# Kernel tuning notes

Hardware: AMD Instinct MI355X
Metric: run time of the kernel (lower is better)

Reference implementation:

```python
import jax, jax.numpy as jnp
import numpy as np
import math

RATIO = 16
B, C, H, W = 8, 684, 16, 64
HID, INP, AD, V, T = 256, 256, 512, 111, 36

def conv2d(x, w, b=None, padding=0):
    out = jax.lax.conv_general_dilated(x, w, (1, 1), [(padding, padding)] * 2,
                                       dimension_numbers=('NCHW', 'OIHW', 'NCHW'))
    if b is not None:
        out = out + b[None, :, None, None]
    return out

def pos_embedding_sine(mask, num_pos_feats=256, temperature=10000.0):
    # mask: [B,H,W] float. Normalized sine position embedding -> [B, 2*num_pos_feats, H, W]
    scale = 2.0 * math.pi
    eps = 1e-6
    y = jnp.cumsum(mask, axis=1)
    x = jnp.cumsum(mask, axis=2)
    y = y / (y[:, -1:, :] + eps) * scale
    x = x / (x[:, :, -1:] + eps) * scale
    i = jnp.arange(num_pos_feats, dtype=jnp.float32)
    dim_t = temperature ** (2.0 * jnp.floor(i / 2.0) / num_pos_feats)
    px = x[..., None] / dim_t  # [B,H,W,F]
    py = y[..., None] / dim_t
    def interleave(p):
        return jnp.stack((jnp.sin(p[..., 0::2]), jnp.cos(p[..., 1::2])), axis=4).reshape(p.shape[:3] + (num_pos_feats,))
    pos = jnp.concatenate((interleave(py), interleave(px)), axis=3)
    return jnp.transpose(pos, (0, 3, 1, 2))

def gru_cell(x, h, w_ih, w_hh, b_ih, b_hh):
    gi = x @ w_ih.T + b_ih
    gh = h @ w_hh.T + b_hh
    ir, iz, inn = jnp.split(gi, 3, axis=-1)
    hr, hz, hn = jnp.split(gh, 3, axis=-1)
    r = jax.nn.sigmoid(ir + hr)
    z = jax.nn.sigmoid(iz + hz)
    n = jnp.tanh(inn + r * hn)
    return (1.0 - z) * n + z * h

def setup_inputs() -> dict:
    key = jax.random.key(0)
    ks = jax.random.split(key, 32)
    s = 0.05
    d = {}
    d['cnn_features'] = jax.random.normal(ks[0], (B, C, H, W), jnp.float32)
    d['counting_preds'] = jax.random.uniform(ks[1], (B, V), jnp.float32)
    d['images_mask'] = jnp.ones((B, 1, H * RATIO, W * RATIO), jnp.float32)
    d['init_W'] = jax.random.normal(ks[2], (HID, C), jnp.float32) * s
    d['init_b'] = jax.random.normal(ks[3], (HID,), jnp.float32) * s
    d['emb'] = jax.random.normal(ks[4], (V, INP), jnp.float32) * s
    d['gru_w_ih'] = jax.random.normal(ks[5], (3 * HID, INP), jnp.float32) * s
    d['gru_w_hh'] = jax.random.normal(ks[6], (3 * HID, HID), jnp.float32) * s
    d['gru_b_ih'] = jax.random.normal(ks[7], (3 * HID,), jnp.float32) * s
    d['gru_b_hh'] = jax.random.normal(ks[8], (3 * HID,), jnp.float32) * s
    d['att_hidden_W'] = jax.random.normal(ks[9], (AD, HID), jnp.float32) * s
    d['att_hidden_b'] = jax.random.normal(ks[10], (AD,), jnp.float32) * s
    d['att_conv_w'] = jax.random.normal(ks[11], (512, 1, 11, 11), jnp.float32) * s
    d['att_weight_W'] = jax.random.normal(ks[12], (AD, 512), jnp.float32) * s
    d['alpha_convert_W'] = jax.random.normal(ks[13], (1, AD), jnp.float32) * s
    d['alpha_convert_b'] = jax.random.normal(ks[14], (1,), jnp.float32) * s
    d['enc_conv_w'] = jax.random.normal(ks[15], (AD, C, 1, 1), jnp.float32) * s
    d['enc_conv_b'] = jax.random.normal(ks[16], (AD,), jnp.float32) * s
    d['state_W'] = jax.random.normal(ks[17], (HID, HID), jnp.float32) * s
    d['state_b'] = jax.random.normal(ks[18], (HID,), jnp.float32) * s
    d['embw_W'] = jax.random.normal(ks[19], (HID, INP), jnp.float32) * s
    d['embw_b'] = jax.random.normal(ks[20], (HID,), jnp.float32) * s
    d['ctx_W'] = jax.random.normal(ks[21], (HID, C), jnp.float32) * s
    d['ctx_b'] = jax.random.normal(ks[22], (HID,), jnp.float32) * s
    d['count_W'] = jax.random.normal(ks[23], (HID, V), jnp.float32) * s
    d['count_b'] = jax.random.normal(ks[24], (HID,), jnp.float32) * s
    d['out_W'] = jax.random.normal(ks[25], (V, HID), jnp.float32) * s
    d['out_b'] = jax.random.normal(ks[26], (V,), jnp.float32) * s
    d['labels'] = jax.random.randint(ks[27], (B, T), 1, V)
    return d

def reference(cnn_features, counting_preds, images_mask, init_W, init_b, emb,
              gru_w_ih, gru_w_hh, gru_b_ih, gru_b_hh,
              att_hidden_W, att_hidden_b, att_conv_w, att_weight_W,
              alpha_convert_W, alpha_convert_b, enc_conv_w, enc_conv_b,
              state_W, state_b, embw_W, embw_b, ctx_W, ctx_b,
              count_W, count_b, out_W, out_b, labels):
    b, c, h, w = cnn_features.shape
    dmask = images_mask[:, :, ::RATIO, ::RATIO]  # [B,1,H,W]
    mask_hw = dmask[:, 0]                        # [B,H,W]
    # init hidden
    avg = jnp.sum(cnn_features * dmask, axis=(2, 3)) / jnp.sum(dmask, axis=(2, 3))
    hidden0 = jnp.tanh(avg @ init_W.T + init_b)
    counting_ctx = counting_preds @ count_W.T + count_b  # [B,HID]
    trans = conv2d(cnn_features, enc_conv_w, enc_conv_b)  # [B,AD,H,W], k=1
    trans = trans + pos_embedding_sine(mask_hw)
    trans_hw = jnp.transpose(trans, (0, 2, 3, 1))  # [B,H,W,AD]
    word0 = jnp.ones((b,), dtype=labels.dtype)
    words_in = jnp.concatenate([word0[:, None], labels[:, :-1]], axis=1)  # teacher forcing
    alpha_sum0 = jnp.zeros((b, 1, h, w), cnn_features.dtype)

    def step(carry, word):
        hidden, alpha_sum = carry
        we = emb[word]
        hidden = gru_cell(we, hidden, gru_w_ih, gru_w_hh, gru_b_ih, gru_b_hh)
        query = hidden @ att_hidden_W.T + att_hidden_b          # [B,AD]
        ast = conv2d(alpha_sum, att_conv_w, padding=5)          # [B,512,H,W]
        coverage = jnp.einsum('bchw,dc->bhwd', ast, att_weight_W)
        score = jnp.tanh(query[:, None, None, :] + coverage + trans_hw)
        energy = jnp.einsum('bhwd,d->bhw', score, alpha_convert_W[0]) + alpha_convert_b[0]
        energy = energy - energy.max()
        e = jnp.exp(energy) * mask_hw
        alpha = e / (jnp.sum(e, axis=(1, 2))[:, None, None] + 1e-10)
        alpha_sum = alpha[:, None] + alpha_sum
        ctx = jnp.einsum('bhw,bchw->bc', alpha, cnn_features)
        out_state = (hidden @ state_W.T + state_b
                     + we @ embw_W.T + embw_b
                     + ctx @ ctx_W.T + ctx_b
                     + counting_ctx)
        prob = out_state @ out_W.T + out_b
        return (hidden, alpha_sum), prob

    _, probs = jax.lax.scan(step, (hidden0, alpha_sum0), words_in.T)
    return jnp.transpose(probs, (1, 0, 2))  # [B,T,V]
```

## Files before the change

### kernel.cpp

```cpp
#include <hip/hip_runtime.h>
#include <hip/hip_bf16.h>
#include <math.h>

#define NB 8
#define NC 684
#define NH 16
#define NW 64
#define NHW 1024
#define NHID 256
#define NAD 512
#define NV 111
#define NT 36
#define KPAD 704

typedef __attribute__((ext_vector_type(8))) short bf16x8;
typedef __attribute__((ext_vector_type(4))) float f32x4;

__device__ __forceinline__ float wred_sum(float v){
  #pragma unroll
  for (int o = 32; o > 0; o >>= 1) v += __shfl_xor(v, o, 64);
  return v;
}
__device__ __forceinline__ float wred_max(float v){
  #pragma unroll
  for (int o = 32; o > 0; o >>= 1) v = fmaxf(v, __shfl_xor(v, o, 64));
  return v;
}
__device__ __forceinline__ float fsig(float x){ return 1.f/(1.f + __expf(-x)); }
__device__ __forceinline__ float ftanh(float x){ float e = __expf(2.f*x); return 1.f - 2.f/(e + 1.f); }
__device__ __forceinline__ unsigned short f2bf(float f){
  __hip_bfloat16 h = __float2bfloat16(f);
  return *(unsigned short*)&h;
}
__device__ __forceinline__ float bf2f(unsigned short u){
  return __uint_as_float(((unsigned)u) << 16);
}

__global__ void k_p0(const float* __restrict__ im, float* __restrict__ dmask,
                     float* __restrict__ msum, float* __restrict__ ys, float* __restrict__ xs,
                     float* __restrict__ idt, float* __restrict__ abuf)
{
  const int tid = threadIdx.x;
  for (int i = tid; i < NB*NHW; i += 256){
    int b = i >> 10, hw = i & 1023; int h = hw >> 6, w = hw & 63;
    dmask[i] = im[b*(256*1024) + (h*16)*1024 + (w*16)];
    abuf[i] = 0.f;
  }
  if (tid < 128) idt[tid] = expf(-(float)tid * (9.210340371976184f/128.f));
  __syncthreads();
  if (tid < 8){
    float s = 0.f;
    for (int i = 0; i < NHW; i++) s += dmask[tid*NHW + i];
    msum[tid] = s;
  }
  for (int p = tid; p < NB*NW; p += 256){
    int b = p >> 6, w = p & 63;
    float tot = 0.f;
    for (int h = 0; h < NH; h++) tot += dmask[b*NHW + h*64 + w];
    float inv = 6.283185307179586f/(tot + 1e-6f);
    float run = 0.f;
    for (int h = 0; h < NH; h++){ run += dmask[b*NHW + h*64 + w]; ys[b*NHW + h*64 + w] = run*inv; }
  }
  for (int p = tid; p < NB*NH; p += 256){
    int b = p >> 4, h = p & 15;
    float tot = 0.f;
    for (int w = 0; w < NW; w++) tot += dmask[b*NHW + h*64 + w];
    float inv = 6.283185307179586f/(tot + 1e-6f);
    float run = 0.f;
    for (int w = 0; w < NW; w++){ run += dmask[b*NHW + h*64 + w]; xs[b*NHW + h*64 + w] = run*inv; }
  }
}

__global__ void k_avg(const float* __restrict__ cnn, const float* __restrict__ dmask,
                      const float* __restrict__ msum, float* __restrict__ avg)
{
  int gid = blockIdx.x*blockDim.x + threadIdx.x;
  int gw = gid >> 6, lane = gid & 63;
  int nw = (gridDim.x*blockDim.x) >> 6;
  for (int ow = gw; ow < NB*NC; ow += nw){
    int b = ow / NC;
    const float* base = cnn + (size_t)ow * NHW;
    const float* dm = dmask + b*NHW;
    float s = 0.f;
    for (int i = lane; i < NHW; i += 64) s += base[i]*dm[i];
    s = wred_sum(s);
    if (lane == 0) avg[ow] = s / msum[b];
  }
}

__global__ void k_init(const float* __restrict__ avg, const float* __restrict__ iW, const float* __restrict__ ib,
                       const float* __restrict__ cp, const float* __restrict__ cW, const float* __restrict__ cb,
                       float* __restrict__ hm1, float* __restrict__ cctx)
{
  int gid = blockIdx.x*blockDim.x + threadIdx.x;
  int gw = gid >> 6, lane = gid & 63;
  int nw = (gridDim.x*blockDim.x) >> 6;
  for (int ow = gw; ow < 2*NB*NHID; ow += nw){
    if (ow < NB*NHID){
      int b = ow >> 8, j = ow & 255;
      float s = 0.f;
      for (int k = lane; k < NC; k += 64) s += avg[b*NC + k]*iW[j*NC + k];
      s = wred_sum(s);
      if (lane == 0) hm1[ow] = tanhf(s + ib[j]);
    } else {
      int o = ow - NB*NHID; int b = o >> 8, j = o & 255;
      float s = 0.f;
      for (int k = lane; k < NV; k += 64) s += cp[b*NV + k]*cW[j*NV + k];
      s = wred_sum(s);
      if (lane == 0) cctx[o] = s + cb[j];
    }
  }
}

__global__ __launch_bounds__(256) void k_cvt(const float* __restrict__ cnn, unsigned short* __restrict__ cnnT)
{
  const int hw0 = blockIdx.x << 6, c0 = blockIdx.y << 6, b = blockIdx.z;
  __shared__ float T[64][65];
  const int tid = threadIdx.x;
  #pragma unroll
  for (int u = 0; u < 16; u++){
    int idx = tid + (u<<8);
    int cc = idx >> 6, mm = idx & 63;
    int c = c0 + cc;
    T[cc][mm] = (c < NC) ? cnn[((size_t)b*NC + c)*NHW + hw0 + mm] : 0.f;
  }
  __syncthreads();
  #pragma unroll
  for (int r0 = 0; r0 < 64; r0 += 8){
    int hwl = r0 + (tid >> 5);
    int cp = (tid & 31) << 1;
    unsigned u0 = f2bf(T[cp][hwl]);
    unsigned u1 = f2bf(T[cp+1][hwl]);
    *(unsigned*)&cnnT[((size_t)((b<<10) + hw0 + hwl))*KPAD + c0 + cp] = (u1 << 16) | u0;
  }
}

__global__ void k_cvtw(const float* __restrict__ ew, unsigned short* __restrict__ ewb)
{
  int x = blockIdx.x*256 + threadIdx.x;
  if (x >= NAD*KPAD) return;
  int d = x / KPAD, c = x - d*KPAD;
  float v = (c < NC) ? ew[(size_t)d*NC + c] : 0.f;
  ewb[x] = f2bf(v);
}

__global__ __launch_bounds__(256) void k_mma_trans(const unsigned short* __restrict__ cnnT,
    const unsigned short* __restrict__ ewb, const float* __restrict__ eb,
    const float* __restrict__ ys, const float* __restrict__ xs,
    const float* __restrict__ idt, unsigned short* __restrict__ transb)
{
  const int m0 = blockIdx.x << 7;
  const int n0 = blockIdx.y << 6;
  const int b = m0 >> 10, hw0 = m0 & 1023;
  const int tid = threadIdx.x, lane = tid & 63, wv = tid >> 6;
  const int kgrp = (lane >> 4) << 3;
  const unsigned short* arow0 = cnnT + ((size_t)((b<<10) + hw0 + (wv<<5) + (lane & 15)))*KPAD + kgrp;
  const unsigned short* arow1 = arow0 + (size_t)16*KPAD;
  f32x4 acc[2][4];
  #pragma unroll
  for (int mt=0; mt<2; mt++)
    #pragma unroll
    for (int s = 0; s < 4; s++){ acc[mt][s][0]=0.f; acc[mt][s][1]=0.f; acc[mt][s][2]=0.f; acc[mt][s][3]=0.f; }
  #pragma unroll 2
  for (int k0 = 0; k0 < KPAD; k0 += 32){
    bf16x8 a0 = *(const bf16x8*)(arow0 + k0);
    bf16x8 a1 = *(const bf16x8*)(arow1 + k0);
    #pragma unroll
    for (int s = 0; s < 4; s++){
      const unsigned short* brow = ewb + (size_t)(n0 + (s<<4) + (lane & 15))*KPAD + kgrp + k0;
      bf16x8 bf = *(const bf16x8*)brow;
      acc[0][s] = __builtin_amdgcn_mfma_f32_16x16x32_bf16(a0, bf, acc[0][s], 0, 0, 0);
      acc[1][s] = __builtin_amdgcn_mfma_f32_16x16x32_bf16(a1, bf, acc[1][s], 0, 0, 0);
    }
  }
  #pragma unroll
  for (int mt = 0; mt < 2; mt++){
    #pragma unroll
    for (int r = 0; r < 4; r++){
      int hw = hw0 + (wv<<5) + (mt<<4) + ((lane>>4)<<2) + r;
      float ysv = ys[(b<<10)+hw], xsv = xs[(b<<10)+hw];
      #pragma unroll
      for (int s = 0; s < 4; s++){
        int d = n0 + (s<<4) + (lane & 15);
        float idtv = (d < 256) ? idt[d>>1] : idt[(d-256)>>1];
        float base = (d < 256) ? ysv : xsv;
        float arg = base*idtv;
        float pe = (d & 1) ? cosf(arg) : sinf(arg);
        transb[((size_t)((b<<10)+hw))*NAD + d] = f2bf(acc[mt][s][r] + eb[d] + pe);
      }
    }
  }
}

__global__ __launch_bounds__(256) void k_wproj(const float* __restrict__ emb, const float* __restrict__ wih,
    const float* __restrict__ bih, const float* __restrict__ ewW, const float* __restrict__ ewb2,
    float* __restrict__ giW, float* __restrict__ embwW)
{
  const int v = blockIdx.x, g = blockIdx.y;
  const int tid = threadIdx.x;
  __shared__ float er[256];
  er[tid] = emb[(size_t)v*256 + tid];
  __syncthreads();
  if (g < 3){
    int i = (g<<8) + tid;
    float s = 0.f;
    const float* wr = wih + (size_t)i*256;
    #pragma unroll 4
    for (int k = 0; k < 256; k++) s += er[k]*wr[k];
    giW[(size_t)v*768 + i] = s + bih[i];
  } else {
    float s = 0.f;
    const float* wr = ewW + (size_t)tid*256;
    #pragma unroll 4
    for (int k = 0; k < 256; k++) s += er[k]*wr[k];
    embwW[(size_t)v*256 + tid] = s + ewb2[tid];
  }
}

__global__ __launch_bounds__(128) void k_ewo(const float* __restrict__ embwW, const float* __restrict__ oW,
                                             float* __restrict__ embwOW)
{
  const int v = blockIdx.x;
  const int u = threadIdx.x;
  __shared__ float ew[256];
  ew[u] = embwW[(size_t)v*256 + u];
  ew[128 + u] = embwW[(size_t)v*256 + 128 + u];
  __syncthreads();
  if (u < NV){
    float s = 0.f;
    const float* wr = oW + (size_t)u*256;
    #pragma unroll 4
    for (int k = 0; k < 256; k++) s += ew[k]*wr[k];
    embwOW[v*NV + u] = s;
  }
}

__global__ void k_mt(const float* __restrict__ aw, const float* __restrict__ acw, unsigned short* __restrict__ MtT)
{
  __shared__ float col[512];
  int t = blockIdx.x; int tid = threadIdx.x;
  for (int c = tid; c < 512; c += 256) col[c] = acw[(size_t)c*121 + t];
  __syncthreads();
  for (int d = tid; d < 512; d += 256){
    float s = 0.f;
    const float4* r4 = (const float4*)(aw + (size_t)d*512);
    for (int k = 0; k < 128; k++){
      float4 w = r4[k];
      s += col[k*4+0]*w.x + col[k*4+1]*w.y + col[k*4+2]*w.z + col[k*4+3]*w.w;
    }
    MtT[d*128 + t] = f2bf(s);
    if (t == 0){
      #pragma unroll
      for (int p = 121; p < 128; p++) MtT[d*128 + p] = 0;
    }
  }
}

__global__ __launch_bounds__(256) void k_so(const float* __restrict__ sW, const float* __restrict__ oW,
    const float* __restrict__ sb, const float* __restrict__ cxb, const float* __restrict__ cctx,
    const float* __restrict__ ob, float* __restrict__ SO, float* __restrict__ CB)
{
  const int v = blockIdx.x; const int tid = threadIdx.x;
  float acc = 0.f;
  for (int j = 0; j < 256; j++) acc += sW[(size_t)j*256 + tid] * oW[(size_t)v*256 + j];
  SO[(size_t)v*256 + tid] = acc;
  if (tid < 8){
    float s = ob[v];
    for (int j = 0; j < 256; j++) s += (sb[j] + cxb[j] + cctx[tid*256 + j]) * oW[(size_t)v*256 + j];
    CB[tid*NV + v] = s;
  }
}

__global__ __launch_bounds__(256) void k_co(const float* __restrict__ cxW, const float* __restrict__ oW,
                                            unsigned short* __restrict__ COb)
{
  const int c = blockIdx.x*256 + threadIdx.x;
  const int v = blockIdx.y;
  if (c >= KPAD) return;
  float acc = 0.f;
  if (v < NV && c < NC){
    for (int j = 0; j < 256; j++) acc += cxW[(size_t)j*NC + c] * oW[(size_t)v*256 + j];
  }
  COb[(size_t)v*KPAD + c] = f2bf(acc);
}

__global__ __launch_bounds__(256) void k_mma_PO(const unsigned short* __restrict__ cnnT,
    const unsigned short* __restrict__ COb, float* __restrict__ PO)
{
  const int m0 = blockIdx.x << 6;
  const int n0 = blockIdx.y << 6;
  const int b = blockIdx.z;
  const int tid = threadIdx.x, lane = tid & 63, wv = tid >> 6;
  const int mrow = m0 + (wv<<4) + (lane & 15);
  const int kgrp = (lane >> 4) << 3;
  const unsigned short* arow = cnnT + ((size_t)((b<<10) + mrow))*KPAD + kgrp;
  f32x4 acc[4];
  #pragma unroll
  for (int s = 0; s < 4; s++){ acc[s][0]=0.f; acc[s][1]=0.f; acc[s][2]=0.f; acc[s][3]=0.f; }
  #pragma unroll 2
  for (int k0 = 0; k0 < KPAD; k0 += 32){
    bf16x8 af = *(const bf16x8*)(arow + k0);
    #pragma unroll
    for (int s = 0; s < 4; s++){
      const unsigned short* brow = COb + (size_t)(n0 + (s<<4) + (lane & 15))*KPAD + kgrp + k0;
      bf16x8 bf = *(const bf16x8*)brow;
      acc[s] = __builtin_amdgcn_mfma_f32_16x16x32_bf16(af, bf, acc[s], 0, 0, 0);
    }
  }
  #pragma unroll
  for (int s = 0; s < 4; s++){
    int v = n0 + (s<<4) + (lane & 15);
    #pragma unroll
    for (int r = 0; r < 4; r++){
      int hw = m0 + (wv<<4) + ((lane>>4)<<2) + r;
      PO[(((size_t)b*128 + v)<<10) + hw] = acc[s][r];
    }
  }
}

__device__ __forceinline__ void gru_slice(const float* __restrict__ hs, const float* __restrict__ whh,
    const float* __restrict__ bhh, const float* __restrict__ gg, float* __restrict__ hdst,
    int r, int wid, int lane)
{
  #pragma unroll 1
  for (int jj = 0; jj < 8; jj++){
    int j = (r<<6) + (wid<<3) + jj;
    float sr = 0.f, sz = 0.f, sn = 0.f;
    #pragma unroll
    for (int u = 0; u < 4; u++){
      int k = lane + (u<<6);
      float hv = hs[k];
      sr += hv * whh[(size_t)j*256 + k];
      sz += hv * whh[(size_t)(j+256)*256 + k];
      sn += hv * whh[(size_t)(j+512)*256 + k];
    }
    sr = wred_sum(sr); sz = wred_sum(sz); sn = wred_sum(sn);
    if (lane == 0){
      float rr = 1.f/(1.f + expf(-(gg[j] + sr + bhh[j])));
      float zz = 1.f/(1.f + expf(-(gg[j+256] + sz + bhh[j+256])));
      float nn = tanhf(gg[j+512] + rr*(sn + bhh[j+512]));
      hdst[j] = (1.f - zz)*nn + zz*hs[j];
    }
  }
}

__global__ __launch_bounds__(512) void k_gq0(const float* __restrict__ hm1, const float* __restrict__ whh,
    const float* __restrict__ bhh, const float* __restrict__ giW, float* __restrict__ hbuf3)
{
  const int r = blockIdx.x, b = blockIdx.y;
  const int tid = threadIdx.x, lane = tid & 63, wid = tid >> 6;
  __shared__ float hs[256];
  if (tid < 256) hs[tid] = hm1[(b<<8) + tid];
  __syncthreads();
  gru_slice(hs, whh, bhh, giW + 768, hbuf3 + (b<<8), r, wid, lane);
}

__global__ void k_tr(const float* __restrict__ whh, const float* __restrict__ ahW,
                     __hip_bfloat162* __restrict__ whhTjb, __hip_bfloat162* __restrict__ ahWTb)
{
  int i = blockIdx.x*256 + threadIdx.x;
  int stride = gridDim.x*256;
  for (int x = i; x < 3*256*128; x += stride){
    int kp = x & 127, j = (x >> 7) & 255, g = x >> 15;
    float lo = whh[(size_t)((g<<8)+j)*256 + (kp<<1)];
    float hi = whh[(size_t)((g<<8)+j)*256 + (kp<<1) + 1];
    __hip_bfloat162 h2; h2.x = __float2bfloat16(lo); h2.y = __float2bfloat16(hi);
    whhTjb[x] = h2;
  }
  for (int x = i; x < 128*512; x += stride){
    int d = x & 511, kp = x >> 9;
    float lo = ahW[(size_t)d*256 + (kp<<1)];
    float hi = ahW[(size_t)d*256 + (kp<<1) + 1];
    __hip_bfloat162 h2; h2.x = __float2bfloat16(lo); h2.y = __float2bfloat16(hi);
    ahWTb[x] = h2;
  }
}

__global__ __launch_bounds__(512) void k_step(
  const float* __restrict__ dmask, const unsigned short* __restrict__ MtT,
  const unsigned short* __restrict__ transb,
  const float* __restrict__ acvW, const float* __restrict__ acvb,
  const float* __restrict__ PO, const float* __restrict__ SO,
  const float* __restrict__ CB, const float* __restrict__ embwOW,
  const float* __restrict__ giW, const int* __restrict__ lab,
  const __hip_bfloat162* __restrict__ whhTjb,
  const float* __restrict__ bhh, const __hip_bfloat162* __restrict__ ahWTb,
  const float* __restrict__ ahb, float* __restrict__ hbuf3,
  float* __restrict__ abuf, float* __restrict__ ebuf,
  float* __restrict__ out, int t)
{
  const int gid = blockIdx.x, tid = threadIdx.x;
  const int lane = tid & 63, wv = tid >> 6;
  const int b = gid >> 5, seg = gid & 31, h = seg >> 1, w0 = (seg & 1) << 5;
  __shared__ float eo[32][516];
  __shared__ float al[1024];
  __shared__ float as4[11][44];
  __shared__ unsigned short Asb[32*136];
  __shared__ float hq[256];
  __shared__ float qs[512];
  __shared__ float red[18];

  const float* eprev = ebuf + (((t+1)&1)<<13);
  float*       ecurb = ebuf + ((t&1)<<13);
  const float* aprev = abuf + (((t+1)&1)<<13);
  float*       acur  = abuf + ((t&1)<<13);

  if (t < NT && tid < 256) hq[tid] = hbuf3[(t%3)*2048 + (b<<8) + tid];

  if (t > 0){
    float e0 = eprev[(b<<10)+tid], e1 = eprev[(b<<10)+512+tid];
    float dm0 = dmask[(b<<10)+tid], dm1 = dmask[(b<<10)+512+tid];
    float m = wred_max(fmaxf(e0, e1));
    if (lane == 0) red[wv] = m;
    __syncthreads();
    if (tid == 0){
      float g = red[0];
      #pragma unroll
      for (int k = 1; k < 8; k++) g = fmaxf(g, red[k]);
      red[16] = g;
    }
    __syncthreads();
    float g = red[16];
    float x0 = __expf(e0 - g)*dm0, x1 = __expf(e1 - g)*dm1;
    float s = wred_sum(x0 + x1);
    if (lane == 0) red[wv] = s;
    __syncthreads();
    if (tid == 0){
      float ss = 0.f;
      #pragma unroll
      for (int k = 0; k < 8; k++) ss += red[k];
      red[17] = ss;
    }
    __syncthreads();
    float inv = 1.f/(red[17] + 1e-10f);
    al[tid] = x0*inv; al[512+tid] = x1*inv;
    __syncthreads();
    if (seg == 0 && t < NT){
      acur[(b<<10)+tid]     = aprev[(b<<10)+tid]     + al[tid];
      acur[(b<<10)+512+tid] = aprev[(b<<10)+512+tid] + al[512+tid];
    }
    if (wv < 4){
      int v = seg + (wv<<5);
      if (v < NV){
        int wprev = (t-1 == 0) ? 1 : lab[b*NT + t - 2];
        const float* POr = PO + (((size_t)b*128 + v)<<10);
        const float* hr = hbuf3 + ((t-1)%3)*2048 + (b<<8);
        const float* SOr = SO + (size_t)v*256;
        float a2 = 0.f;
        #pragma unroll
        for (int u = 0; u < 16; u++){ int p = lane + (u<<6); a2 += al[p]*POr[p]; }
        #pragma unroll
        for (int u = 0; u < 4; u++){ int k = lane + (u<<6); a2 += hr[k]*SOr[k]; }
        a2 = wred_sum(a2);
        if (lane == 0)
          out[((size_t)b*NT + (t-1))*NV + v] = a2 + CB[b*NV + v] + embwOW[wprev*NV + v];
      }
    }
  }
  if (t < NT){
    for (int idx = tid; idx < 11*44; idx += 512){
      int r = idx/44, c = idx - r*44;
      float v = 0.f;
      if (t > 0 && c < 42){
        int hi2 = h + r - 5, wi = w0 + c - 5;
        if ((unsigned)hi2 < 16u && (unsigned)wi < 64u){
          int p = (hi2<<6) + wi;
          v = aprev[(b<<10)+p] + al[p];
        }
      }
      as4[r][c] = v;
    }
    {
      float s2 = 0.f;
      #pragma unroll 4
      for (int kp = 0; kp < 128; kp++){
        __hip_bfloat162 w = ahWTb[(kp<<9) + tid];
        s2 += hq[kp<<1]*__bfloat162float(w.x) + hq[(kp<<1)+1]*__bfloat162float(w.y);
      }
      qs[tid] = s2 + ahb[tid];
    }
    __syncthreads();
    #pragma unroll
    for (int u = 0; u < 8; u++){
      int idx = tid + (u<<9);
      int w = idx >> 7, tap = idx & 127;
      float v = 0.f;
      if (tap < 121 && t > 0){
        int ki = tap/11, kj = tap - ki*11;
        v = as4[ki][w + kj];
      }
      Asb[w*136 + tap] = f2bf(v);
    }
    __syncthreads();
    const int mh = wv & 1, ns = wv >> 1;
    const int kg = (lane >> 4) << 3;
    f32x4 acc[8];
    #pragma unroll
    for (int s = 0; s < 8; s++){ acc[s][0]=0.f; acc[s][1]=0.f; acc[s][2]=0.f; acc[s][3]=0.f; }
    if (t > 0){
      const unsigned short* ab = &Asb[((mh<<4) + (lane & 15))*136 + kg];
      #pragma unroll
      for (int k0 = 0; k0 < 128; k0 += 32){
        bf16x8 af = *(const bf16x8*)(ab + k0);
        #pragma unroll
        for (int s = 0; s < 8; s++){
          const unsigned short* brow = MtT + (size_t)((ns<<7) + (s<<4) + (lane & 15))*128 + kg + k0;
          bf16x8 bf = *(const bf16x8*)brow;
          acc[s] = __builtin_amdgcn_mfma_f32_16x16x32_bf16(af, bf, acc[s], 0, 0, 0);
        }
      }
    }
    const float acb0 = acvb[0];
    #pragma unroll
    for (int s = 0; s < 8; s++){
      int d = (ns<<7) + (s<<4) + (lane & 15);
      float wav = acvW[d];
      float qd = qs[d];
      #pragma unroll
      for (int r = 0; r < 4; r++){
        int w = (mh<<4) + ((lane>>4)<<2) + r;
        int hw = (h<<6) + w0 + w;
        float tv = bf2f(transb[((size_t)((b<<10)+hw))*NAD + d]);
        eo[w][d] = wav * ftanh(qd + tv + acc[s][r]);
      }
    }
    __syncthreads();
    float* ecur = ecurb + (b<<10) + (h<<6) + w0;
    #pragma unroll
    for (int k = 0; k < 4; k++){
      int w = (wv<<2) + k;
      float sum = 0.f;
      #pragma unroll
      for (int u = 0; u < 8; u++) sum += eo[w][lane + (u<<6)];
      sum = wred_sum(sum);
      if (lane == 0) ecur[w] = sum + acb0;
    }
    if (seg < 8 && t < NT-1){
      int j = (seg<<5) + (wv<<2) + (lane>>4);
      int qg = lane & 15;
      const __hip_bfloat162* r0 = whhTjb + (size_t)j*128 + (qg<<3);
      const __hip_bfloat162* r1 = whhTjb + (size_t)(256+j)*128 + (qg<<3);
      const __hip_bfloat162* r2 = whhTjb + (size_t)(512+j)*128 + (qg<<3);
      float sr = 0.f, sz = 0.f, sn = 0.f;
      #pragma unroll
      for (int i = 0; i < 8; i++){
        int kp = (qg<<3) + i;
        float h0 = hq[kp<<1], h1 = hq[(kp<<1)+1];
        __hip_bfloat162 wr = r0[i], wz2 = r1[i], wn = r2[i];
        sr += h0*__bfloat162float(wr.x) + h1*__bfloat162float(wr.y);
        sz += h0*__bfloat162float(wz2.x) + h1*__bfloat162float(wz2.y);
        sn += h0*__bfloat162float(wn.x) + h1*__bfloat162float(wn.y);
      }
      #pragma unroll
      for (int o = 1; o < 16; o <<= 1){
        sr += __shfl_xor(sr, o, 64);
        sz += __shfl_xor(sz, o, 64);
        sn += __shfl_xor(sn, o, 64);
      }
      if (qg == 0){
        int wnext = lab[b*NT + t];
        const float* gg = giW + (size_t)wnext*768;
        float r = fsig(gg[j] + sr + bhh[j]);
        float z = fsig(gg[j+256] + sz + bhh[j+256]);
        float n = ftanh(gg[j+512] + r*(sn + bhh[j+512]));
        hbuf3[((t+1)%3)*2048 + (b<<8) + j] = (1.f - z)*n + z*hq[j];
      }
    }
  }
}

extern "C" void kernel_launch(void* const* d_in, const int* in_sizes, int n_in,
                              void* d_out, int out_size, void* d_ws, size_t ws_size,
                              hipStream_t stream)
{
  const float* cnn  = (const float*)d_in[0];
  const float* cp   = (const float*)d_in[1];
  const float* im   = (const float*)d_in[2];
  const float* iW   = (const float*)d_in[3];
  const float* ib   = (const float*)d_in[4];
  const float* emb  = (const float*)d_in[5];
  const float* wih  = (const float*)d_in[6];
  const float* whh  = (const float*)d_in[7];
  const float* bih  = (const float*)d_in[8];
  const float* bhh  = (const float*)d_in[9];
  const float* ahW  = (const float*)d_in[10];
  const float* ahb  = (const float*)d_in[11];
  const float* acw  = (const float*)d_in[12];
  const float* awW  = (const float*)d_in[13];
  const float* acvW = (const float*)d_in[14];
  const float* acvb = (const float*)d_in[15];
  const float* ecw  = (const float*)d_in[16];
  const float* ecb  = (const float*)d_in[17];
  const float* sW   = (const float*)d_in[18];
  const float* sb   = (const float*)d_in[19];
  const float* ewW  = (const float*)d_in[20];
  const float* ewb2 = (const float*)d_in[21];
  const float* cxW  = (const float*)d_in[22];
  const float* cxb  = (const float*)d_in[23];
  const float* cW   = (const float*)d_in[24];
  const float* cb   = (const float*)d_in[25];
  const float* oW   = (const float*)d_in[26];
  const float* ob   = (const float*)d_in[27];
  const int*   lab  = (const int*)d_in[28];
  float* out = (float*)d_out;
  float* ws = (float*)d_ws;

  float* dmask  = ws + 0;
  float* ys     = ws + 8192;
  float* xs     = ws + 16384;
  float* idt    = ws + 24576;
  float* msum   = ws + 24704;
  float* avg    = ws + 24720;
  float* cctx   = ws + 30192;
  float* hm1    = ws + 32240;
  float* hbuf3  = ws + 34288;
  float* abuf   = ws + 40432;
  float* ebuf   = ws + 56816;
  float* giW    = ws + 73200;
  float* embwW  = ws + 158448;
  float* embwOW = ws + 186864;
  unsigned short* MtT = (unsigned short*)(ws + 199216);
  float* SO     = ws + 231984;
  float* CB     = ws + 260400;
  __hip_bfloat162* whhTjb = (__hip_bfloat162*)(ws + 261296);
  __hip_bfloat162* ahWTb  = (__hip_bfloat162*)(ws + 359600);
  unsigned short* cnnT = (unsigned short*)(ws + 425136);
  unsigned short* ewbb = (unsigned short*)(ws + 3308720);
  unsigned short* COb  = (unsigned short*)(ws + 3488944);
  unsigned short* transb = (unsigned short*)(ws + 3534000);
  float* PO     = ws + 5631152;

  k_p0<<<1, 256, 0, stream>>>(im, dmask, msum, ys, xs, idt, abuf);
  k_avg<<<456, 256, 0, stream>>>(cnn, dmask, msum, avg);
  k_init<<<256, 256, 0, stream>>>(avg, iW, ib, cp, cW, cb, hm1, cctx);
  k_wproj<<<dim3(NV, 4), 256, 0, stream>>>(emb, wih, bih, ewW, ewb2, giW, embwW);
  k_ewo<<<NV, 128, 0, stream>>>(embwW, oW, embwOW);
  k_cvt<<<dim3(16, 11, 8), 256, 0, stream>>>(cnn, cnnT);
  k_cvtw<<<(NAD*KPAD + 255)/256, 256, 0, stream>>>(ecw, ewbb);
  k_mma_trans<<<dim3(64, 8), 256, 0, stream>>>(cnnT, ewbb, ecb, ys, xs, idt, transb);
  k_mt<<<121, 256, 0, stream>>>(awW, acw, MtT);
  k_so<<<NV, 256, 0, stream>>>(sW, oW, sb, cxb, cctx, ob, SO, CB);
  k_co<<<dim3(3, 128), 256, 0, stream>>>(cxW, oW, COb);
  k_mma_PO<<<dim3(16, 2, 8), 256, 0, stream>>>(cnnT, COb, PO);
  k_tr<<<128, 256, 0, stream>>>(whh, ahW, whhTjb, ahWTb);
  k_gq0<<<dim3(4, 8), 512, 0, stream>>>(hm1, whh, bhh, giW, hbuf3);

  for (int t = 0; t <= NT; t++){
    k_step<<<256, 512, 0, stream>>>(dmask, MtT, transb, acvW, acvb, PO, SO, CB, embwOW,
                                    giW, lab, whhTjb, bhh, ahWTb, ahb, hbuf3, abuf, ebuf, out, t);
  }
}
```

Measured before the change: 1.068 ms.

## Split step kernel into 512 smaller blocks and stage trans output through LDS

```diff
diff --git a/kernel.cpp b/kernel.cpp
--- a/kernel.cpp
+++ b/kernel.cpp
@@ -153,6 +153,7 @@
   const int n0 = blockIdx.y << 6;
   const int b = m0 >> 10, hw0 = m0 & 1023;
   const int tid = threadIdx.x, lane = tid & 63, wv = tid >> 6;
+  __shared__ unsigned short ts[128*66];
   const int kgrp = (lane >> 4) << 3;
   const unsigned short* arow0 = cnnT + ((size_t)((b<<10) + hw0 + (wv<<5) + (lane & 15)))*KPAD + kgrp;
   const unsigned short* arow1 = arow0 + (size_t)16*KPAD;
@@ -177,7 +178,8 @@
   for (int mt = 0; mt < 2; mt++){
     #pragma unroll
     for (int r = 0; r < 4; r++){
-      int hw = hw0 + (wv<<5) + (mt<<4) + ((lane>>4)<<2) + r;
+      int l = (wv<<5) + (mt<<4) + ((lane>>4)<<2) + r;
+      int hw = hw0 + l;
       float ysv = ys[(b<<10)+hw], xsv = xs[(b<<10)+hw];
       #pragma unroll
       for (int s = 0; s < 4; s++){
@@ -186,9 +188,18 @@
         float base = (d < 256) ? ysv : xsv;
         float arg = base*idtv;
         float pe = (d & 1) ? cosf(arg) : sinf(arg);
-        transb[((size_t)((b<<10)+hw))*NAD + d] = f2bf(acc[mt][s][r] + eb[d] + pe);
-      }
-    }
+        ts[l*66 + (s<<4) + (lane & 15)] = f2bf(acc[mt][s][r] + eb[d] + pe);
+      }
+    }
+  }
+  __syncthreads();
+  const unsigned* ts32 = (const unsigned*)ts;
+  unsigned* dst32 = (unsigned*)transb;
+  #pragma unroll
+  for (int k = 0; k < 16; k++){
+    int i = tid + (k<<8);
+    int row = i >> 5, col = i & 31;
+    dst32[((size_t)((b<<10) + hw0 + row))*256 + (n0>>1) + col] = ts32[row*33 + col];
   }
 }
 
@@ -356,7 +367,7 @@
 }
 
 __global__ void k_tr(const float* __restrict__ whh, const float* __restrict__ ahW,
-                     __hip_bfloat162* __restrict__ whhTjb, __hip_bfloat162* __restrict__ ahWTb)
+                     __hip_bfloat162* __restrict__ whhTjb, unsigned short* __restrict__ ahWTr)
 {
   int i = blockIdx.x*256 + threadIdx.x;
   int stride = gridDim.x*256;
@@ -367,16 +378,12 @@
     __hip_bfloat162 h2; h2.x = __float2bfloat16(lo); h2.y = __float2bfloat16(hi);
     whhTjb[x] = h2;
   }
-  for (int x = i; x < 128*512; x += stride){
-    int d = x & 511, kp = x >> 9;
-    float lo = ahW[(size_t)d*256 + (kp<<1)];
-    float hi = ahW[(size_t)d*256 + (kp<<1) + 1];
-    __hip_bfloat162 h2; h2.x = __float2bfloat16(lo); h2.y = __float2bfloat16(hi);
-    ahWTb[x] = h2;
-  }
-}
-
-__global__ __launch_bounds__(512) void k_step(
+  for (int x = i; x < 512*256; x += stride){
+    ahWTr[x] = f2bf(ahW[x]);
+  }
+}
+
+__global__ __launch_bounds__(256) void k_step(
   const float* __restrict__ dmask, const unsigned short* __restrict__ MtT,
   const unsigned short* __restrict__ transb,
   const float* __restrict__ acvW, const float* __restrict__ acvb,
@@ -384,62 +391,63 @@
   const float* __restrict__ CB, const float* __restrict__ embwOW,
   const float* __restrict__ giW, const int* __restrict__ lab,
   const __hip_bfloat162* __restrict__ whhTjb,
-  const float* __restrict__ bhh, const __hip_bfloat162* __restrict__ ahWTb,
+  const float* __restrict__ bhh, const unsigned short* __restrict__ ahWTr,
   const float* __restrict__ ahb, float* __restrict__ hbuf3,
   float* __restrict__ abuf, float* __restrict__ ebuf,
   float* __restrict__ out, int t)
 {
   const int gid = blockIdx.x, tid = threadIdx.x;
   const int lane = tid & 63, wv = tid >> 6;
-  const int b = gid >> 5, seg = gid & 31, h = seg >> 1, w0 = (seg & 1) << 5;
-  __shared__ float eo[32][516];
+  const int b = gid >> 6, seg = gid & 63, h = seg >> 2, w0 = (seg & 3) << 4;
+  __shared__ float eo[16][516];
   __shared__ float al[1024];
-  __shared__ float as4[11][44];
-  __shared__ unsigned short Asb[32*136];
+  __shared__ float as4[11][28];
+  __shared__ unsigned short Asb[16*136];
   __shared__ float hq[256];
   __shared__ float qs[512];
-  __shared__ float red[18];
+  __shared__ float red[10];
 
   const float* eprev = ebuf + (((t+1)&1)<<13);
   float*       ecurb = ebuf + ((t&1)<<13);
   const float* aprev = abuf + (((t+1)&1)<<13);
   float*       acur  = abuf + ((t&1)<<13);
 
-  if (t < NT && tid < 256) hq[tid] = hbuf3[(t%3)*2048 + (b<<8) + tid];
+  if (t < NT) hq[tid] = hbuf3[(t%3)*2048 + (b<<8) + tid];
 
   if (t > 0){
-    float e0 = eprev[(b<<10)+tid], e1 = eprev[(b<<10)+512+tid];
-    float dm0 = dmask[(b<<10)+tid], dm1 = dmask[(b<<10)+512+tid];
-    float m = wred_max(fmaxf(e0, e1));
+    float e[4], dm[4];
+    #pragma unroll
+    for (int k = 0; k < 4; k++){
+      e[k] = eprev[(b<<10) + tid + (k<<8)];
+      dm[k] = dmask[(b<<10) + tid + (k<<8)];
+    }
+    float m = fmaxf(fmaxf(e[0], e[1]), fmaxf(e[2], e[3]));
+    m = wred_max(m);
     if (lane == 0) red[wv] = m;
     __syncthreads();
-    if (tid == 0){
-      float g = red[0];
-      #pragma unroll
-      for (int k = 1; k < 8; k++) g = fmaxf(g, red[k]);
-      red[16] = g;
-    }
-    __syncthreads();
-    float g = red[16];
-    float x0 = __expf(e0 - g)*dm0, x1 = __expf(e1 - g)*dm1;
-    float s = wred_sum(x0 + x1);
+    if (tid == 0) red[8] = fmaxf(fmaxf(red[0], red[1]), fmaxf(red[2], red[3]));
+    __syncthreads();
+    float g = red[8];
+    float x[4]; float s = 0.f;
+    #pragma unroll
+    for (int k = 0; k < 4; k++){ x[k] = __expf(e[k] - g)*dm[k]; s += x[k]; }
+    s = wred_sum(s);
     if (lane == 0) red[wv] = s;
     __syncthreads();
-    if (tid == 0){
-      float ss = 0.f;
-      #pragma unroll
-      for (int k = 0; k < 8; k++) ss += red[k];
-      red[17] = ss;
-    }
-    __syncthreads();
-    float inv = 1.f/(red[17] + 1e-10f);
-    al[tid] = x0*inv; al[512+tid] = x1*inv;
+    if (tid == 0) red[9] = red[0] + red[1] + red[2] + red[3];
+    __syncthreads();
+    float inv = 1.f/(red[9] + 1e-10f);
+    #pragma unroll
+    for (int k = 0; k < 4; k++) al[tid + (k<<8)] = x[k]*inv;
     __syncthreads();
     if (seg == 0 && t < NT){
-      acur[(b<<10)+tid]     = aprev[(b<<10)+tid]     + al[tid];
-      acur[(b<<10)+512+tid] = aprev[(b<<10)+512+tid] + al[512+tid];
-    }
-    if (wv < 4){
+      #pragma unroll
+      for (int k = 0; k < 4; k++){
+        int p = tid + (k<<8);
+        acur[(b<<10)+p] = aprev[(b<<10)+p] + al[p];
+      }
+    }
+    if (seg < 32){
       int v = seg + (wv<<5);
       if (v < NV){
         int wprev = (t-1 == 0) ? 1 : lab[b*NT + t - 2];
@@ -458,10 +466,10 @@
     }
   }
   if (t < NT){
-    for (int idx = tid; idx < 11*44; idx += 512){
-      int r = idx/44, c = idx - r*44;
+    for (int idx = tid; idx < 11*28; idx += 256){
+      int r = idx/28, c = idx - r*28;
       float v = 0.f;
-      if (t > 0 && c < 42){
+      if (t > 0 && c < 26){
         int hi2 = h + r - 5, wi = w0 + c - 5;
         if ((unsigned)hi2 < 16u && (unsigned)wi < 64u){
           int p = (hi2<<6) + wi;
@@ -471,18 +479,27 @@
       as4[r][c] = v;
     }
     {
-      float s2 = 0.f;
-      #pragma unroll 4
-      for (int kp = 0; kp < 128; kp++){
-        __hip_bfloat162 w = ahWTb[(kp<<9) + tid];
-        s2 += hq[kp<<1]*__bfloat162float(w.x) + hq[(kp<<1)+1]*__bfloat162float(w.y);
-      }
-      qs[tid] = s2 + ahb[tid];
+      const unsigned short* ar0 = ahWTr + (size_t)tid*256;
+      const unsigned short* ar1 = ahWTr + (size_t)(tid+256)*256;
+      float s0 = 0.f, s1 = 0.f;
+      #pragma unroll 8
+      for (int g8 = 0; g8 < 32; g8++){
+        bf16x8 wa = *(const bf16x8*)(ar0 + (g8<<3));
+        bf16x8 wb = *(const bf16x8*)(ar1 + (g8<<3));
+        #pragma unroll
+        for (int i = 0; i < 8; i++){
+          float hv = hq[(g8<<3) + i];
+          s0 += hv*bf2f((unsigned short)wa[i]);
+          s1 += hv*bf2f((unsigned short)wb[i]);
+        }
+      }
+      qs[tid] = s0 + ahb[tid];
+      qs[tid+256] = s1 + ahb[tid+256];
     }
     __syncthreads();
     #pragma unroll
     for (int u = 0; u < 8; u++){
-      int idx = tid + (u<<9);
+      int idx = tid + (u<<8);
       int w = idx >> 7, tap = idx & 127;
       float v = 0.f;
       if (tap < 121 && t > 0){
@@ -492,19 +509,18 @@
       Asb[w*136 + tap] = f2bf(v);
     }
     __syncthreads();
-    const int mh = wv & 1, ns = wv >> 1;
     const int kg = (lane >> 4) << 3;
     f32x4 acc[8];
     #pragma unroll
     for (int s = 0; s < 8; s++){ acc[s][0]=0.f; acc[s][1]=0.f; acc[s][2]=0.f; acc[s][3]=0.f; }
     if (t > 0){
-      const unsigned short* ab = &Asb[((mh<<4) + (lane & 15))*136 + kg];
+      const unsigned short* ab = &Asb[(lane & 15)*136 + kg];
       #pragma unroll
       for (int k0 = 0; k0 < 128; k0 += 32){
         bf16x8 af = *(const bf16x8*)(ab + k0);
         #pragma unroll
         for (int s = 0; s < 8; s++){
-          const unsigned short* brow = MtT + (size_t)((ns<<7) + (s<<4) + (lane & 15))*128 + kg + k0;
+          const unsigned short* brow = MtT + (size_t)((wv<<7) + (s<<4) + (lane & 15))*128 + kg + k0;
           bf16x8 bf = *(const bf16x8*)brow;
           acc[s] = __builtin_amdgcn_mfma_f32_16x16x32_bf16(af, bf, acc[s], 0, 0, 0);
         }
@@ -513,12 +529,12 @@
     const float acb0 = acvb[0];
     #pragma unroll
     for (int s = 0; s < 8; s++){
-      int d = (ns<<7) + (s<<4) + (lane & 15);
+      int d = (wv<<7) + (s<<4) + (lane & 15);
       float wav = acvW[d];
       float qd = qs[d];
       #pragma unroll
       for (int r = 0; r < 4; r++){
-        int w = (mh<<4) + ((lane>>4)<<2) + r;
+        int w = ((lane>>4)<<2) + r;
         int hw = (h<<6) + w0 + w;
         float tv = bf2f(transb[((size_t)((b<<10)+hw))*NAD + d]);
         eo[w][d] = wav * ftanh(qd + tv + acc[s][r]);
@@ -535,8 +551,8 @@
       sum = wred_sum(sum);
       if (lane == 0) ecur[w] = sum + acb0;
     }
-    if (seg < 8 && t < NT-1){
-      int j = (seg<<5) + (wv<<2) + (lane>>4);
+    if (seg < 16 && t < NT-1){
+      int j = (seg<<4) + (wv<<2) + (lane>>4);
       int qg = lane & 15;
       const __hip_bfloat162* r0 = whhTjb + (size_t)j*128 + (qg<<3);
       const __hip_bfloat162* r1 = whhTjb + (size_t)(256+j)*128 + (qg<<3);
@@ -623,7 +639,7 @@
   float* SO     = ws + 231984;
   float* CB     = ws + 260400;
   __hip_bfloat162* whhTjb = (__hip_bfloat162*)(ws + 261296);
-  __hip_bfloat162* ahWTb  = (__hip_bfloat162*)(ws + 359600);
+  unsigned short* ahWTr  = (unsigned short*)(ws + 359600);
   unsigned short* cnnT = (unsigned short*)(ws + 425136);
   unsigned short* ewbb = (unsigned short*)(ws + 3308720);
   unsigned short* COb  = (unsigned short*)(ws + 3488944);
@@ -642,11 +658,11 @@
   k_so<<<NV, 256, 0, stream>>>(sW, oW, sb, cxb, cctx, ob, SO, CB);
   k_co<<<dim3(3, 128), 256, 0, stream>>>(cxW, oW, COb);
   k_mma_PO<<<dim3(16, 2, 8), 256, 0, stream>>>(cnnT, COb, PO);
-  k_tr<<<128, 256, 0, stream>>>(whh, ahW, whhTjb, ahWTb);
+  k_tr<<<128, 256, 0, stream>>>(whh, ahW, whhTjb, ahWTr);
   k_gq0<<<dim3(4, 8), 512, 0, stream>>>(hm1, whh, bhh, giW, hbuf3);
 
   for (int t = 0; t <= NT; t++){
-    k_step<<<256, 512, 0, stream>>>(dmask, MtT, transb, acvW, acvb, PO, SO, CB, embwOW,
-                                    giW, lab, whhTjb, bhh, ahWTb, ahb, hbuf3, abuf, ebuf, out, t);
-  }
-}
+    k_step<<<512, 256, 0, stream>>>(dmask, MtT, transb, acvW, acvb, PO, SO, CB, embwOW,
+                                    giW, lab, whhTjb, bhh, ahWTr, ahb, hbuf3, abuf, ebuf, out, t);
+  }
+}
```

Result: slower. 1.321 ms (+23.7%).

## Precompute softmax partial sums in producer step, drop max-subtraction reductions

Applied to the files above, without the earlier changes.

```diff
diff --git a/kernel.cpp b/kernel.cpp
--- a/kernel.cpp
+++ b/kernel.cpp
@@ -19,11 +19,6 @@
 __device__ __forceinline__ float wred_sum(float v){
   #pragma unroll
   for (int o = 32; o > 0; o >>= 1) v += __shfl_xor(v, o, 64);
-  return v;
-}
-__device__ __forceinline__ float wred_max(float v){
-  #pragma unroll
-  for (int o = 32; o > 0; o >>= 1) v = fmaxf(v, __shfl_xor(v, o, 64));
   return v;
 }
 __device__ __forceinline__ float fsig(float x){ return 1.f/(1.f + __expf(-x)); }
@@ -387,7 +382,7 @@
   const float* __restrict__ bhh, const __hip_bfloat162* __restrict__ ahWTb,
   const float* __restrict__ ahb, float* __restrict__ hbuf3,
   float* __restrict__ abuf, float* __restrict__ ebuf,
-  float* __restrict__ out, int t)
+  float* __restrict__ esumP, float* __restrict__ out, int t)
 {
   const int gid = blockIdx.x, tid = threadIdx.x;
   const int lane = tid & 63, wv = tid >> 6;
@@ -398,7 +393,7 @@
   __shared__ unsigned short Asb[32*136];
   __shared__ float hq[256];
   __shared__ float qs[512];
-  __shared__ float red[18];
+  __shared__ float part[8];
 
   const float* eprev = ebuf + (((t+1)&1)<<13);
   float*       ecurb = ebuf + ((t&1)<<13);
@@ -408,32 +403,17 @@
   if (t < NT && tid < 256) hq[tid] = hbuf3[(t%3)*2048 + (b<<8) + tid];
 
   if (t > 0){
+    float ssum = 1e-10f;
+    {
+      const float* ep = esumP + ((t-1)%3)*256 + (b<<5);
+      #pragma unroll
+      for (int k = 0; k < 32; k++) ssum += ep[k];
+    }
+    const float inv = 1.f/ssum;
     float e0 = eprev[(b<<10)+tid], e1 = eprev[(b<<10)+512+tid];
     float dm0 = dmask[(b<<10)+tid], dm1 = dmask[(b<<10)+512+tid];
-    float m = wred_max(fmaxf(e0, e1));
-    if (lane == 0) red[wv] = m;
-    __syncthreads();
-    if (tid == 0){
-      float g = red[0];
-      #pragma unroll
-      for (int k = 1; k < 8; k++) g = fmaxf(g, red[k]);
-      red[16] = g;
-    }
-    __syncthreads();
-    float g = red[16];
-    float x0 = __expf(e0 - g)*dm0, x1 = __expf(e1 - g)*dm1;
-    float s = wred_sum(x0 + x1);
-    if (lane == 0) red[wv] = s;
-    __syncthreads();
-    if (tid == 0){
-      float ss = 0.f;
-      #pragma unroll
-      for (int k = 0; k < 8; k++) ss += red[k];
-      red[17] = ss;
-    }
-    __syncthreads();
-    float inv = 1.f/(red[17] + 1e-10f);
-    al[tid] = x0*inv; al[512+tid] = x1*inv;
+    al[tid] = __expf(e0)*dm0*inv;
+    al[512+tid] = __expf(e1)*dm1*inv;
     __syncthreads();
     if (seg == 0 && t < NT){
       acur[(b<<10)+tid]     = aprev[(b<<10)+tid]     + al[tid];
@@ -526,6 +506,7 @@
     }
     __syncthreads();
     float* ecur = ecurb + (b<<10) + (h<<6) + w0;
+    float pe = 0.f;
     #pragma unroll
     for (int k = 0; k < 4; k++){
       int w = (wv<<2) + k;
@@ -533,7 +514,19 @@
       #pragma unroll
       for (int u = 0; u < 8; u++) sum += eo[w][lane + (u<<6)];
       sum = wred_sum(sum);
-      if (lane == 0) ecur[w] = sum + acb0;
+      if (lane == 0){
+        float ev = sum + acb0;
+        ecur[w] = ev;
+        pe += __expf(ev)*dmask[(b<<10) + (h<<6) + w0 + w];
+      }
+    }
+    if (lane == 0) part[wv] = pe;
+    __syncthreads();
+    if (tid == 0){
+      float tp = 0.f;
+      #pragma unroll
+      for (int k = 0; k < 8; k++) tp += part[k];
+      esumP[(t%3)*256 + (b<<5) + seg] = tp;
     }
     if (seg < 8 && t < NT-1){
       int j = (seg<<5) + (wv<<2) + (lane>>4);
@@ -629,6 +622,7 @@
   unsigned short* COb  = (unsigned short*)(ws + 3488944);
   unsigned short* transb = (unsigned short*)(ws + 3534000);
   float* PO     = ws + 5631152;
+  float* esumP  = ws + 9825456;
 
   k_p0<<<1, 256, 0, stream>>>(im, dmask, msum, ys, xs, idt, abuf);
   k_avg<<<456, 256, 0, stream>>>(cnn, dmask, msum, avg);
@@ -647,6 +641,7 @@
 
   for (int t = 0; t <= NT; t++){
     k_step<<<256, 512, 0, stream>>>(dmask, MtT, transb, acvW, acvb, PO, SO, CB, embwOW,
-                                    giW, lab, whhTjb, bhh, ahWTb, ahb, hbuf3, abuf, ebuf, out, t);
-  }
-}
+                                    giW, lab, whhTjb, bhh, ahWTb, ahb, hbuf3, abuf, ebuf,
+                                    esumP, out, t);
+  }
+}
```

New measurement: 1.065 ms. Within noise of the previous version (-0.3%).
